# Performance work log

Hardware: AMD Instinct MI355X
Metric: run time of the kernel (lower is better)

The kernel has to match this reference:

```python
import jax, jax.numpy as jnp
import numpy as np

B, D, S, K, A = 4096, 256, 32, 8192, 256
BETA = 0.25  # vq_commitment_beta


def _ln(x, g, b):
    m = jnp.mean(x, axis=-1, keepdims=True)
    v = jnp.var(x, axis=-1, keepdims=True)
    return (x - m) * jax.lax.rsqrt(v + 1e-5) * g + b


def _clin(zr, zi, Wr, Wi, br, bi):
    # torch ComplexLinear: real = Wr(zr) - Wi(zi); imag = Wi(zr) + Wr(zi)
    return (zr @ Wr.T + br) - (zi @ Wi.T + bi), (zr @ Wi.T + bi) + (zi @ Wr.T + br)


def _forward(x_t_r, x_t_i, gw_r, gw_i, mem_r, mem_i, input_gate, vq_emb,
             vis_pal, aud_pal, mem_gate_W, mem_gate_b, mem_addr_W, mem_addr_b,
             mn_gr, mn_br, mn_gi, mn_bi,
             gq_Wr, gq_Wi, gq_br, gq_bi, gk_Wr, gk_Wi, gk_br, gk_bi,
             gv_Wr, gv_Wi, gv_br, gv_bi, sp_Wr, sp_Wi, sp_br, sp_bi,
             cr_Wr, cr_Wi, cr_br, cr_bi):
    # input gate blend (forward_step preamble)
    alpha = jax.nn.sigmoid(input_gate)
    gr = alpha * gw_r + (1.0 - alpha) * x_t_r
    gi = alpha * gw_i + (1.0 - alpha) * x_t_i
    z_flat = jnp.concatenate([gr, gi], -1)  # [B, 2D]

    # ---- EMA_VQ (eval path): cdist + argmin + straight-through ----
    d2 = (jnp.sum(z_flat ** 2, 1, keepdims=True) + jnp.sum(vq_emb ** 2, 1)
          - 2.0 * (z_flat @ vq_emb.T))  # [B, K]
    idx = jnp.argmin(d2, -1)
    z_q = vq_emb[idx]
    vq_loss = BETA * jnp.mean((jax.lax.stop_gradient(z_q) - z_flat) ** 2, -1)
    v_out = z_flat + jax.lax.stop_gradient(z_q - z_flat)
    probs = jnp.mean(jax.nn.one_hot(idx, K, dtype=jnp.float32), 0)
    batch_ent = -jnp.sum(probs * jnp.log(probs + 1e-10)) / jnp.log(jnp.asarray(K, jnp.float32))

    # ---- HermitianGating ----
    qr, qi = _clin(gr, gi, gq_Wr, gq_Wi, gq_br, gq_bi)
    kr, ki = _clin(gr, gi, gk_Wr, gk_Wi, gk_br, gk_bi)
    vr, vi = _clin(gr, gi, gv_Wr, gv_Wi, gv_br, gv_bi)
    gate = jax.nn.sigmoid(jnp.sum(qr * kr + qi * ki, -1, keepdims=True))  # Re(q k*)
    g_out = jnp.concatenate([vr * gate, vi * gate], -1)

    # ---- AssociativeMemory: content read + gated soft-scatter write ----
    sim = jnp.einsum('bsd,bd->bs', mem_r, gr) + jnp.einsum('bsd,bd->bs', mem_i, gi)  # Re(mem* q)
    attn = jax.nn.softmax(sim, -1)
    read_r = jnp.einsum('bs,bsd->bd', attn, mem_r)
    read_i = jnp.einsum('bs,bsd->bd', attn, mem_i)
    m_out = jnp.concatenate([read_r, read_i], -1)
    wgate = jax.nn.sigmoid(z_flat @ mem_gate_W.T + mem_gate_b)  # [B,1]
    ww = jax.nn.softmax(z_flat @ mem_addr_W.T + mem_addr_b, -1)  # [B,S]
    slot_ent = jnp.mean(-jnp.sum(ww * jnp.log(ww + 1e-10), -1))
    eff = wgate[:, :, None] * ww[:, :, None]  # [B,S,1]
    nm_r = _ln((1.0 - eff) * mem_r + eff * gr[:, None, :], mn_gr, mn_br)
    nm_i = _ln((1.0 - eff) * mem_i + eff * gi[:, None, :], mn_gi, mn_bi)

    # ---- HebbianSensory palette attention ----
    sr, si = _clin(gr, gi, sp_Wr, sp_Wi, sp_br, sp_bi)
    zf2 = jnp.concatenate([sr, si], -1)
    vis_attn = jax.nn.softmax(zf2 @ vis_pal.T, -1)
    aud_attn = jax.nn.softmax(zf2 @ aud_pal.T, -1)
    vis = vis_attn @ vis_pal
    aud = aud_attn @ aud_pal
    # experience = vis_c + i*aud_c
    s_out = jnp.concatenate([vis[:, :D] - aud[:, D:], vis[:, D:] + aud[:, :D]], -1)

    # ---- Critic: i * ComplexLinear(z) ----
    c_r, c_i = _clin(gr, gi, cr_Wr, cr_Wi, cr_br, cr_bi)
    c_out = jnp.concatenate([-c_i, c_r], -1)

    out_main = jnp.stack([v_out, g_out, m_out, s_out, c_out], 1)  # [B,5,2D]
    return out_main, nm_r, nm_i, idx, vq_loss, batch_ent, slot_ent


def setup_inputs():
    key = jax.random.key(0)
    ks = iter(jax.random.split(key, 48))
    n = lambda shape, s=1.0: jax.random.normal(next(ks), shape, dtype=jnp.float32) * s
    inp = {
        'x_t_r': n((B, D)), 'x_t_i': n((B, D)),
        'gw_r': n((B, D)), 'gw_i': n((B, D)),
        'mem_r': n((B, S, D)), 'mem_i': n((B, S, D)),
        'input_gate': jnp.zeros((), jnp.float32),
        'vq_emb': jax.random.uniform(next(ks), (K, 2 * D), jnp.float32, -1.0 / np.sqrt(D), 1.0 / np.sqrt(D)),
        'vis_pal': n((A, 2 * D)), 'aud_pal': n((A, 2 * D)),
        'mem_gate_W': n((1, 2 * D), 0.02), 'mem_gate_b': jnp.zeros((1,), jnp.float32),
        'mem_addr_W': n((S, 2 * D), 0.02), 'mem_addr_b': jnp.zeros((S,), jnp.float32),
        'mn_gr': jnp.ones((D,), jnp.float32), 'mn_br': jnp.zeros((D,), jnp.float32),
        'mn_gi': jnp.ones((D,), jnp.float32), 'mn_bi': jnp.zeros((D,), jnp.float32),
    }
    for p in ('gq', 'gk', 'gv', 'sp', 'cr'):
        inp[p + '_Wr'] = n((D, D), 0.05)
        inp[p + '_Wi'] = n((D, D), 0.05)
        inp[p + '_br'] = jnp.zeros((D,), jnp.float32)
        inp[p + '_bi'] = jnp.zeros((D,), jnp.float32)
    return inp


def reference(x_t_r, x_t_i, gw_r, gw_i, mem_r, mem_i, input_gate, vq_emb,
              vis_pal, aud_pal, mem_gate_W, mem_gate_b, mem_addr_W, mem_addr_b,
              mn_gr, mn_br, mn_gi, mn_bi,
              gq_Wr, gq_Wi, gq_br, gq_bi, gk_Wr, gk_Wi, gk_br, gk_bi,
              gv_Wr, gv_Wi, gv_br, gv_bi, sp_Wr, sp_Wi, sp_br, sp_bi,
              cr_Wr, cr_Wi, cr_br, cr_bi):
    return _forward(x_t_r, x_t_i, gw_r, gw_i, mem_r, mem_i, input_gate, vq_emb,
                    vis_pal, aud_pal, mem_gate_W, mem_gate_b, mem_addr_W, mem_addr_b,
                    mn_gr, mn_br, mn_gi, mn_bi,
                    gq_Wr, gq_Wi, gq_br, gq_bi, gk_Wr, gk_Wi, gk_br, gk_bi,
                    gv_Wr, gv_Wi, gv_br, gv_bi, sp_Wr, sp_Wi, sp_br, sp_bi,
                    cr_Wr, cr_Wi, cr_br, cr_bi)
```

## Files before the change

### kernel.cpp

```cpp
#include <hip/hip_runtime.h>
#include <hip/hip_bf16.h>
#include <math.h>

#define BN 4096
#define DN 256
#define SN 32
#define KN 8192
#define AN 256
#define TWO_D 512

typedef unsigned short ushort;
using bf16x8 = __attribute__((ext_vector_type(8))) short;
using f32x4  = __attribute__((ext_vector_type(4))) float;

#define OUT_MAIN 0ull
#define OUT_NMR  10485760ull
#define OUT_NMI  44040192ull
#define OUT_IDX  77594624ull
#define OUT_VQL  77598720ull
#define OUT_BENT 77602816ull
#define OUT_SENT 77602817ull

#define MBYTE (1024ull*1024ull)
#define WS_GR    (0ull)
#define WS_GI    (4ull*MBYTE)
#define WS_Z2H   (8ull*MBYTE)
#define WS_Z2L   (12ull*MBYTE)
#define WS_EH    (16ull*MBYTE)
#define WS_EL    (24ull*MBYTE)
#define WS_E2    (32ull*MBYTE)
#define WS_WBIG  (33ull*MBYTE)
#define WS_BIAS  (36ull*MBYTE)
#define WS_PALC  (37ull*MBYTE)
#define WS_VIST  (38ull*MBYTE)
#define WS_AUDT  (39ull*MBYTE)
#define WS_PVAL  (40ull*MBYTE)
#define WS_PIDX  (42ull*MBYTE)
#define WS_HIST  (44ull*MBYTE)
#define WS_ENTV  (44ull*MBYTE + 128ull*1024ull)
#define WS_CL    (45ull*MBYTE)
#define WS_LOGIT (65ull*MBYTE)
#define WS_ATTN  (73ull*MBYTE)
#define WS_VIS   (77ull*MBYTE)
#define WS_AUD   (85ull*MBYTE)

#define DEVINL __device__ __forceinline__

DEVINL ushort f2bf(float f) {
    union { float f; unsigned u; } v; v.f = f;
    unsigned r = v.u + 0x7fffu + ((v.u >> 16) & 1u);
    return (ushort)(r >> 16);
}
DEVINL float bf2f(ushort h) {
    union { unsigned u; float f; } v; v.u = ((unsigned)h) << 16;
    return v.f;
}
DEVINL float sigmoidf_(float x) { return 1.f / (1.f + __expf(-x)); }

__global__ __launch_bounds__(256) void k_prep_vq(const float* __restrict__ emb,
                                                 ushort* __restrict__ eh,
                                                 ushort* __restrict__ el,
                                                 float* __restrict__ e2) {
    int t = threadIdx.x, w = t >> 6, lane = t & 63;
    int row = blockIdx.x * 4 + w;
    const float* er = emb + (size_t)row * 512;
    float acc = 0.f;
    #pragma unroll
    for (int j = 0; j < 8; j++) {
        int k = lane + 64 * j;
        float e = er[k];
        ushort h = f2bf(e);
        eh[(size_t)row * 512 + k] = h;
        el[(size_t)row * 512 + k] = f2bf(e - bf2f(h));
        acc += e * e;
    }
    for (int m = 1; m < 64; m <<= 1) acc += __shfl_xor(acc, m, 64);
    if (lane == 0) e2[row] = acc;
}

__global__ void k_prep_wbig(const float* __restrict__ Wr, const float* __restrict__ Wi,
                            const float* __restrict__ br, const float* __restrict__ bi,
                            ushort* __restrict__ Wb, float* __restrict__ bias) {
    int idx = blockIdx.x * 256 + threadIdx.x;
    int j = idx >> 9, k = idx & 511;
    int part = j >> 8, jj = j & 255;
    float v;
    if (part == 0) v = (k < 256) ? Wr[jj * 256 + k] : -Wi[jj * 256 + (k - 256)];
    else           v = (k < 256) ? Wi[jj * 256 + k] :  Wr[jj * 256 + (k - 256)];
    Wb[idx] = f2bf(v);
    if (k == 0) bias[j] = part ? (br[jj] + bi[jj]) : (br[jj] - bi[jj]);
}

__global__ void k_prep_palcat(const float* __restrict__ vis, const float* __restrict__ aud,
                              ushort* __restrict__ palc) {
    int idx = blockIdx.x * 256 + threadIdx.x;
    int a = idx >> 9, k = idx & 511;
    float v = (a < 256) ? vis[a * 512 + k] : aud[(a - 256) * 512 + k];
    palc[idx] = f2bf(v);
}
__global__ void k_prep_palT(const float* __restrict__ vis, const float* __restrict__ aud,
                            ushort* __restrict__ visT, ushort* __restrict__ audT) {
    int idx = blockIdx.x * 256 + threadIdx.x;
    int j = idx >> 8, a = idx & 255;
    visT[j * 256 + a] = f2bf(vis[a * 512 + j]);
    audT[j * 256 + a] = f2bf(aud[a * 512 + j]);
}

__global__ void k_gate(const float* __restrict__ xr, const float* __restrict__ xi,
                       const float* __restrict__ gwr, const float* __restrict__ gwi,
                       const float* __restrict__ ig,
                       float* __restrict__ gr, float* __restrict__ gi,
                       ushort* __restrict__ z2h, ushort* __restrict__ z2l) {
    int i = blockIdx.x * 256 + threadIdx.x;
    float a = sigmoidf_(ig[0]);
    float r  = a * gwr[i] + (1.f - a) * xr[i];
    float im = a * gwi[i] + (1.f - a) * xi[i];
    gr[i] = r; gi[i] = im;
    int b = i >> 8, d = i & 255;
    size_t z = (size_t)b * 512;
    ushort rh = f2bf(r);  z2h[z + d] = rh;       z2l[z + d] = f2bf(r - bf2f(rh));
    ushort ih = f2bf(im); z2h[z + 256 + d] = ih; z2l[z + 256 + d] = f2bf(im - bf2f(ih));
}

__global__ __launch_bounds__(256) void k_vq_gemm(
    const ushort* __restrict__ Zh, const ushort* __restrict__ Zl,
    const ushort* __restrict__ Eh, const ushort* __restrict__ El,
    const float* __restrict__ e2, float* __restrict__ pval, int* __restrict__ pidx) {
    __shared__ ushort Ah[128 * 40], Al[128 * 40], Bh[128 * 40], Bl[128 * 40];
    const int m0 = blockIdx.y * 128, n0 = blockIdx.x * 128;
    const int t = threadIdx.x;
    const int w = t >> 6, lane = t & 63, q = lane >> 4, ln = lane & 15;
    const int wm = w >> 1, wn = w & 1;
    f32x4 acc[4][4] = {};
    const int lrow = t >> 2, lcol = (t & 3) * 8;
    for (int k0 = 0; k0 < 512; k0 += 32) {
        __syncthreads();
        #pragma unroll
        for (int rep = 0; rep < 2; rep++) {
            int r = lrow + rep * 64;
            *(uint4*)(&Ah[r * 40 + lcol]) = *(const uint4*)(Zh + (size_t)(m0 + r) * 512 + k0 + lcol);
            *(uint4*)(&Al[r * 40 + lcol]) = *(const uint4*)(Zl + (size_t)(m0 + r) * 512 + k0 + lcol);
            *(uint4*)(&Bh[r * 40 + lcol]) = *(const uint4*)(Eh + (size_t)(n0 + r) * 512 + k0 + lcol);
            *(uint4*)(&Bl[r * 40 + lcol]) = *(const uint4*)(El + (size_t)(n0 + r) * 512 + k0 + lcol);
        }
        __syncthreads();
        bf16x8 ah[4], al[4], bh[4], bl[4];
        #pragma unroll
        for (int i = 0; i < 4; i++) {
            int ar = wm * 64 + i * 16 + ln;
            ah[i] = *(const bf16x8*)(&Ah[ar * 40 + q * 8]);
            al[i] = *(const bf16x8*)(&Al[ar * 40 + q * 8]);
            int br = wn * 64 + i * 16 + ln;
            bh[i] = *(const bf16x8*)(&Bh[br * 40 + q * 8]);
            bl[i] = *(const bf16x8*)(&Bl[br * 40 + q * 8]);
        }
        #pragma unroll
        for (int i = 0; i < 4; i++)
            #pragma unroll
            for (int j = 0; j < 4; j++) {
                acc[i][j] = __builtin_amdgcn_mfma_f32_16x16x32_bf16(ah[i], bh[j], acc[i][j], 0, 0, 0);
                acc[i][j] = __builtin_amdgcn_mfma_f32_16x16x32_bf16(ah[i], bl[j], acc[i][j], 0, 0, 0);
                acc[i][j] = __builtin_amdgcn_mfma_f32_16x16x32_bf16(al[i], bh[j], acc[i][j], 0, 0, 0);
            }
    }
    float e2v[4]; int cidx[4];
    #pragma unroll
    for (int j = 0; j < 4; j++) { cidx[j] = n0 + wn * 64 + j * 16 + ln; e2v[j] = e2[cidx[j]]; }
    #pragma unroll
    for (int i = 0; i < 4; i++) {
        #pragma unroll
        for (int reg = 0; reg < 4; reg++) {
            float bv = 3.4e38f; int bc = 0x7fffffff;
            #pragma unroll
            for (int j = 0; j < 4; j++) {
                float s = e2v[j] - 2.f * acc[i][j][reg];
                if (s < bv || (s == bv && cidx[j] < bc)) { bv = s; bc = cidx[j]; }
            }
            for (int m = 1; m < 16; m <<= 1) {
                float ov = __shfl_xor(bv, m, 64);
                int   oc = __shfl_xor(bc, m, 64);
                if (ov < bv || (ov == bv && oc < bc)) { bv = ov; bc = oc; }
            }
            if (ln == 0) {
                int r = m0 + wm * 64 + i * 16 + q * 4 + reg;
                int slot = blockIdx.x * 2 + wn;
                pval[(size_t)r * 128 + slot] = bv;
                pidx[(size_t)r * 128 + slot] = bc;
            }
        }
    }
}

__global__ __launch_bounds__(256) void k_vqfin(
    const float* __restrict__ pval, const int* __restrict__ pidx,
    const float* __restrict__ emb, const float* __restrict__ gr,
    const float* __restrict__ gi, float* __restrict__ out, int* __restrict__ hist) {
    __shared__ float sz[512];
    __shared__ float sv[128];
    __shared__ int   scd[128];
    __shared__ int   topc[8];
    __shared__ double tsc[8];
    __shared__ int   sbc;
    int b = blockIdx.x, t = threadIdx.x;
    sz[t]       = gr[(size_t)b * 256 + t];
    sz[256 + t] = gi[(size_t)b * 256 + t];
    if (t < 128) { sv[t] = pval[(size_t)b * 128 + t]; scd[t] = pidx[(size_t)b * 128 + t]; }
    __syncthreads();
    if (t == 0) {
        for (int j = 0; j < 8; j++) {
            float bv = 3.4e38f; int bi = 0;
            for (int m = 0; m < 128; m++) {
                float v = sv[m];
                if (v < bv || (v == bv && scd[m] < scd[bi])) { bv = v; bi = m; }
            }
            topc[j] = scd[bi];
            sv[bi] = 3.4e38f;
        }
    }
    __syncthreads();
    int w = t >> 6, lane = t & 63;
    for (int rep = 0; rep < 2; rep++) {
        int j = w + rep * 4;
        int c = topc[j];
        const float* e = emb + (size_t)c * 512;
        double acc = 0.0;
        #pragma unroll
        for (int u = 0; u < 8; u++) {
            int k2 = lane + u * 64;
            double d = (double)sz[k2] - (double)e[k2];
            acc += d * d;
        }
        for (int m = 1; m < 64; m <<= 1) acc += __shfl_xor(acc, m, 64);
        if (lane == 0) tsc[j] = acc;
    }
    __syncthreads();
    if (t == 0) {
        double bv = tsc[0]; int bc = topc[0];
        for (int j = 1; j < 8; j++)
            if (tsc[j] < bv || (tsc[j] == bv && topc[j] < bc)) { bv = tsc[j]; bc = topc[j]; }
        sbc = bc;
        out[OUT_IDX + b] = (float)bc;
        out[OUT_VQL + b] = (float)(0.25 * bv / 512.0);
        atomicAdd(&hist[bc], 1);
    }
    __syncthreads();
    const float* e = emb + (size_t)sbc * 512;
    float* om = out + (size_t)b * 2560;
    om[t]       = e[t];
    om[256 + t] = e[256 + t];
}

__global__ __launch_bounds__(256) void k_gemm(
    const ushort* __restrict__ A, int lda,
    const ushort* __restrict__ Bm, int ldb,
    void* __restrict__ C, int ldc,
    int Kd, const float* __restrict__ bias, int obf) {
    __shared__ ushort As[128 * 40], Bs[128 * 40];
    const int m0 = blockIdx.y * 128, n0 = blockIdx.x * 128;
    const int t = threadIdx.x;
    const int w = t >> 6, lane = t & 63, q = lane >> 4, ln = lane & 15;
    const int wm = w >> 1, wn = w & 1;
    f32x4 acc[4][4] = {};
    const int lrow = t >> 2, lcol = (t & 3) * 8;
    for (int k0 = 0; k0 < Kd; k0 += 32) {
        __syncthreads();
        #pragma unroll
        for (int rep = 0; rep < 2; rep++) {
            int r = lrow + rep * 64;
            *(uint4*)(&As[r * 40 + lcol]) = *(const uint4*)(A + (size_t)(m0 + r) * lda + k0 + lcol);
            *(uint4*)(&Bs[r * 40 + lcol]) = *(const uint4*)(Bm + (size_t)(n0 + r) * ldb + k0 + lcol);
        }
        __syncthreads();
        bf16x8 af[4], bfr[4];
        #pragma unroll
        for (int i = 0; i < 4; i++) {
            af[i]  = *(const bf16x8*)(&As[(wm * 64 + i * 16 + ln) * 40 + q * 8]);
            bfr[i] = *(const bf16x8*)(&Bs[(wn * 64 + i * 16 + ln) * 40 + q * 8]);
        }
        #pragma unroll
        for (int i = 0; i < 4; i++)
            #pragma unroll
            for (int j = 0; j < 4; j++)
                acc[i][j] = __builtin_amdgcn_mfma_f32_16x16x32_bf16(af[i], bfr[j], acc[i][j], 0, 0, 0);
    }
    #pragma unroll
    for (int i = 0; i < 4; i++) {
        int r = m0 + wm * 64 + i * 16 + q * 4;
        #pragma unroll
        for (int j = 0; j < 4; j++) {
            int c = n0 + wn * 64 + j * 16 + ln;
            float bb = bias ? bias[c] : 0.f;
            #pragma unroll
            for (int reg = 0; reg < 4; reg++) {
                float v = acc[i][j][reg] + bb;
                if (obf) ((ushort*)C)[(size_t)(r + reg) * ldc + c] = f2bf(v);
                else     ((float*)C)[(size_t)(r + reg) * ldc + c] = v;
            }
        }
    }
}

__global__ __launch_bounds__(256) void k_hermit(const ushort* __restrict__ CL,
                                                float* __restrict__ out) {
    int b = blockIdx.x, t = threadIdx.x;
    const ushort* row = CL + (size_t)b * 2560;
    float qr = bf2f(row[t]), qi = bf2f(row[256 + t]);
    float kr = bf2f(row[512 + t]), ki = bf2f(row[768 + t]);
    float part = qr * kr + qi * ki;
    __shared__ float red[4];
    for (int m = 1; m < 64; m <<= 1) part += __shfl_xor(part, m, 64);
    if ((t & 63) == 0) red[t >> 6] = part;
    __syncthreads();
    float gate = sigmoidf_(red[0] + red[1] + red[2] + red[3]);
    float vr = bf2f(row[1024 + t]), vi = bf2f(row[1280 + t]);
    float* om = out + (size_t)b * 2560;
    om[512 + t] = vr * gate; om[512 + 256 + t] = vi * gate;
    float crr = bf2f(row[2048 + t]), cii = bf2f(row[2304 + t]);
    om[4 * 512 + t] = -cii; om[4 * 512 + 256 + t] = crr;
}

__global__ __launch_bounds__(256) void k_smax(const float* __restrict__ L,
                                              ushort* __restrict__ attn) {
    int b = blockIdx.x, t = threadIdx.x;
    __shared__ float sred[8];
    for (int h = 0; h < 2; h++) {
        float x = L[(size_t)b * 512 + h * 256 + t];
        float mx = x;
        for (int m = 1; m < 64; m <<= 1) mx = fmaxf(mx, __shfl_xor(mx, m, 64));
        if ((t & 63) == 0) sred[t >> 6] = mx;
        __syncthreads();
        mx = fmaxf(fmaxf(sred[0], sred[1]), fmaxf(sred[2], sred[3]));
        float e = __expf(x - mx);
        float su = e;
        for (int m = 1; m < 64; m <<= 1) su += __shfl_xor(su, m, 64);
        if ((t & 63) == 0) sred[4 + (t >> 6)] = su;
        __syncthreads();
        su = sred[4] + sred[5] + sred[6] + sred[7];
        attn[(size_t)b * 512 + h * 256 + t] = f2bf(e / su);
        __syncthreads();
    }
}

__global__ void k_sout(const float* __restrict__ vis, const float* __restrict__ aud,
                       float* __restrict__ out) {
    int i = blockIdx.x * 256 + threadIdx.x;
    int b = i >> 8, d = i & 255;
    const float* v = vis + (size_t)b * 512;
    const float* a = aud + (size_t)b * 512;
    float* om = out + (size_t)b * 2560 + 3 * 512;
    om[d]       = v[d] - a[256 + d];
    om[256 + d] = v[256 + d] + a[d];
}

DEVINL void ln_half(float (&v)[32], float zz,
                    const float* __restrict__ gam, const float* __restrict__ bet,
                    float* __restrict__ obase, int t, int wp, int hs,
                    float (*redA)[33], float (*redB)[33],
                    float* __restrict__ smn, float* __restrict__ srs,
                    const float* __restrict__ seff) {
    float keepU = 0.f, keepQ = 0.f;
    #pragma unroll
    for (int s = 0; s < 32; s++) {
        float eff = seff[s];
        float x = v[s] + eff * (zz - v[s]);
        v[s] = x;
        float su = x, sq = x * x;
        #pragma unroll
        for (int m = 1; m <= 16; m <<= 1) {
            su += __shfl_xor(su, m, 64);
            sq += __shfl_xor(sq, m, 64);
        }
        if (hs == s) { keepU = su; keepQ = sq; }
    }
    redA[wp][hs] = keepU;
    redB[wp][hs] = keepQ;
    __syncthreads();
    if (t < 32) {
        float su = 0.f, sq = 0.f;
        #pragma unroll
        for (int j = 0; j < 8; j++) { su += redA[j][t]; sq += redB[j][t]; }
        float mn = su * (1.f / 256.f);
        float va = sq * (1.f / 256.f) - mn * mn;
        smn[t] = mn; srs[t] = rsqrtf(va + 1e-5f);
    }
    __syncthreads();
    float gv = gam[t], bv = bet[t];
    #pragma unroll
    for (int s = 0; s < 32; s++)
        obase[(size_t)s * 256 + t] = (v[s] - smn[s]) * srs[s] * gv + bv;
    __syncthreads();
}

__global__ __launch_bounds__(256, 4) void k_mem(
    const float* __restrict__ mem_r, const float* __restrict__ mem_i,
    const float* __restrict__ gr, const float* __restrict__ gi,
    const float* __restrict__ gateW, const float* __restrict__ gateB,
    const float* __restrict__ addrW, const float* __restrict__ addrB,
    const float* __restrict__ mgr, const float* __restrict__ mbr,
    const float* __restrict__ mgi, const float* __restrict__ mbi,
    float* __restrict__ out, float* __restrict__ entv) {
    __shared__ float redA[8][33];
    __shared__ float redB[8][33];
    __shared__ float redG[8];
    __shared__ float satt[32], seff[32], smn[32], srs[32];
    const int b = blockIdx.x, t = threadIdx.x;
    const int w = t >> 6, lane = t & 63;
    const int wp = (w << 1) | (lane >> 5);
    const int hs = lane & 31;
    const float* mr = mem_r + (size_t)b * 8192;
    const float* mi = mem_i + (size_t)b * 8192;
    const float zr = gr[(size_t)b * 256 + t];
    const float zi = gi[(size_t)b * 256 + t];

    float vr_[32], vi_[32];
    #pragma unroll
    for (int s = 0; s < 32; s++) vr_[s] = mr[s * 256 + t];
    #pragma unroll
    for (int s = 0; s < 32; s++) vi_[s] = mi[s * 256 + t];

    {
        float keepS = 0.f;
        #pragma unroll
        for (int s = 0; s < 32; s++) {
            float ps = vr_[s] * zr + vi_[s] * zi;
            #pragma unroll
            for (int m = 1; m <= 16; m <<= 1) ps += __shfl_xor(ps, m, 64);
            if (hs == s) keepS = ps;
        }
        redA[wp][hs] = keepS;
    }
    {
        float keepW = 0.f;
        #pragma unroll 4
        for (int s = 0; s < 32; s++) {
            float pw = addrW[s * 512 + t] * zr + addrW[s * 512 + 256 + t] * zi;
            #pragma unroll
            for (int m = 1; m <= 16; m <<= 1) pw += __shfl_xor(pw, m, 64);
            if (hs == s) keepW = pw;
        }
        redB[wp][hs] = keepW;
    }
    {
        float pg = gateW[t] * zr + gateW[256 + t] * zi;
        #pragma unroll
        for (int m = 1; m <= 16; m <<= 1) pg += __shfl_xor(pg, m, 64);
        if (hs == 0) redG[wp] = pg;
    }
    __syncthreads();

    if (t < 32) {
        float sim = 0.f, wwl = addrB[t], g = gateB[0];
        #pragma unroll
        for (int j = 0; j < 8; j++) { sim += redA[j][t]; wwl += redB[j][t]; g += redG[j]; }
        float wg = sigmoidf_(g);
        float mx = sim;
        #pragma unroll
        for (int m = 1; m <= 16; m <<= 1) mx = fmaxf(mx, __shfl_xor(mx, m, 64));
        float e = __expf(sim - mx), su = e;
        #pragma unroll
        for (int m = 1; m <= 16; m <<= 1) su += __shfl_xor(su, m, 64);
        satt[t] = e / su;
        mx = wwl;
        #pragma unroll
        for (int m = 1; m <= 16; m <<= 1) mx = fmaxf(mx, __shfl_xor(mx, m, 64));
        e = __expf(wwl - mx); su = e;
        #pragma unroll
        for (int m = 1; m <= 16; m <<= 1) su += __shfl_xor(su, m, 64);
        float wv = e / su;
        seff[t] = wg * wv;
        float ent = -wv * __logf(wv + 1e-10f);
        #pragma unroll
        for (int m = 1; m <= 16; m <<= 1) ent += __shfl_xor(ent, m, 64);
        if (t == 0) entv[b] = ent;
    }
    __syncthreads();

    {
        float rr = 0.f, ri = 0.f;
        #pragma unroll
        for (int s = 0; s < 32; s++) { float a = satt[s]; rr += a * vr_[s]; ri += a * vi_[s]; }
        float* om = out + (size_t)b * 2560 + 1024;
        om[t] = rr; om[256 + t] = ri;
    }

    ln_half(vr_, zr, mgr, mbr, out + OUT_NMR + (size_t)b * 8192,
            t, wp, hs, redA, redB, smn, srs, seff);
    ln_half(vi_, zi, mgi, mbi, out + OUT_NMI + (size_t)b * 8192,
            t, wp, hs, redA, redB, smn, srs, seff);
}

__global__ __launch_bounds__(256) void k_scalars(const int* __restrict__ hist,
                                                 const float* __restrict__ entv,
                                                 float* __restrict__ out) {
    int t = threadIdx.x;
    float local = 0.f;
    for (int k = t; k < 8192; k += 256) {
        float p = (float)hist[k] * (1.f / 4096.f);
        local += -p * __logf(p + 1e-10f);
    }
    float se = 0.f;
    for (int k = t; k < 4096; k += 256) se += entv[k];
    __shared__ float red[4], red2[4];
    for (int m = 1; m < 64; m <<= 1) {
        local += __shfl_xor(local, m, 64);
        se    += __shfl_xor(se, m, 64);
    }
    if ((t & 63) == 0) { red[t >> 6] = local; red2[t >> 6] = se; }
    __syncthreads();
    if (t == 0) {
        float bent = (red[0] + red[1] + red[2] + red[3]) / logf(8192.f);
        out[OUT_BENT] = bent;
        out[OUT_SENT] = (red2[0] + red2[1] + red2[2] + red2[3]) * (1.f / 4096.f);
    }
}

extern "C" void kernel_launch(void* const* d_in, const int* in_sizes, int n_in,
                              void* d_out, int out_size, void* d_ws, size_t ws_size,
                              hipStream_t stream) {
    const float* x_t_r = (const float*)d_in[0];
    const float* x_t_i = (const float*)d_in[1];
    const float* gw_r  = (const float*)d_in[2];
    const float* gw_i  = (const float*)d_in[3];
    const float* mem_r = (const float*)d_in[4];
    const float* mem_i = (const float*)d_in[5];
    const float* ig    = (const float*)d_in[6];
    const float* emb   = (const float*)d_in[7];
    const float* visp  = (const float*)d_in[8];
    const float* audp  = (const float*)d_in[9];
    const float* gateW = (const float*)d_in[10];
    const float* gateB = (const float*)d_in[11];
    const float* addrW = (const float*)d_in[12];
    const float* addrB = (const float*)d_in[13];
    const float* mgr   = (const float*)d_in[14];
    const float* mbr   = (const float*)d_in[15];
    const float* mgi   = (const float*)d_in[16];
    const float* mbi   = (const float*)d_in[17];

    char* w = (char*)d_ws;
    float*  gr    = (float*)(w + WS_GR);
    float*  gi    = (float*)(w + WS_GI);
    ushort* z2h   = (ushort*)(w + WS_Z2H);
    ushort* z2l   = (ushort*)(w + WS_Z2L);
    ushort* eh    = (ushort*)(w + WS_EH);
    ushort* el    = (ushort*)(w + WS_EL);
    float*  e2    = (float*)(w + WS_E2);
    ushort* Wbig  = (ushort*)(w + WS_WBIG);
    float*  biasv = (float*)(w + WS_BIAS);
    ushort* palc  = (ushort*)(w + WS_PALC);
    ushort* visT  = (ushort*)(w + WS_VIST);
    ushort* audT  = (ushort*)(w + WS_AUDT);
    float*  pval  = (float*)(w + WS_PVAL);
    int*    pidx  = (int*)(w + WS_PIDX);
    int*    hist  = (int*)(w + WS_HIST);
    float*  entv  = (float*)(w + WS_ENTV);
    ushort* CLb   = (ushort*)(w + WS_CL);
    float*  logit = (float*)(w + WS_LOGIT);
    ushort* attn  = (ushort*)(w + WS_ATTN);
    float*  vis   = (float*)(w + WS_VIS);
    float*  aud   = (float*)(w + WS_AUD);
    float*  out   = (float*)d_out;

    hipMemsetAsync(w + WS_HIST, 0, 8192 * sizeof(int), stream);

    k_prep_vq<<<KN / 4, 256, 0, stream>>>(emb, eh, el, e2);
    for (int p = 0; p < 5; p++) {
        k_prep_wbig<<<1024, 256, 0, stream>>>(
            (const float*)d_in[18 + p * 4], (const float*)d_in[19 + p * 4],
            (const float*)d_in[20 + p * 4], (const float*)d_in[21 + p * 4],
            Wbig + (size_t)p * 512 * 512, biasv + p * 512);
    }
    k_prep_palcat<<<1024, 256, 0, stream>>>(visp, audp, palc);
    k_prep_palT<<<512, 256, 0, stream>>>(visp, audp, visT, audT);

    k_gate<<<BN, 256, 0, stream>>>(x_t_r, x_t_i, gw_r, gw_i, ig, gr, gi, z2h, z2l);

    k_vq_gemm<<<dim3(64, 32), 256, 0, stream>>>(z2h, z2l, eh, el, e2, pval, pidx);
    k_vqfin<<<BN, 256, 0, stream>>>(pval, pidx, emb, gr, gi, out, hist);

    k_gemm<<<dim3(20, 32), 256, 0, stream>>>(z2h, 512, Wbig, 512, CLb, 2560, 512, biasv, 1);
    k_hermit<<<BN, 256, 0, stream>>>(CLb, out);

    k_gemm<<<dim3(4, 32), 256, 0, stream>>>(CLb + 1536, 2560, palc, 512, logit, 512, 512, nullptr, 0);
    k_smax<<<BN, 256, 0, stream>>>(logit, attn);
    k_gemm<<<dim3(4, 32), 256, 0, stream>>>(attn, 512, visT, 256, vis, 512, 256, nullptr, 0);
    k_gemm<<<dim3(4, 32), 256, 0, stream>>>(attn + 256, 512, audT, 256, aud, 512, 256, nullptr, 0);
    k_sout<<<BN, 256, 0, stream>>>(vis, aud, out);

    k_mem<<<BN, 256, 0, stream>>>(mem_r, mem_i, gr, gi, gateW, gateB, addrW, addrB,
                                  mgr, mbr, mgi, mbi, out, entv);

    k_scalars<<<1, 256, 0, stream>>>(hist, entv, out);
}
```

Before: 1.071 ms.

## Replace per-slot butterfly reductions in k_mem with transposing fold32 reduction

Replaces the 32 independent 5-step shuffle reductions per slot with a recursive-halving transpose-fold that reduces 32 values across the wave in about 32 shuffles, leaving each lane holding one bit-reversed slot sum. Softmax, entropy and the layernorm statistics are then computed redundantly in every wave and broadcast with readlane, which removes the single-warp serial stage and one barrier per layernorm half. The aim is to cut shuffle count and synchronization in the memory-update kernel. In exchange it adds register pressure from the temp arrays and readlane-based indexing.

```diff
diff --git a/kernel.cpp b/kernel.cpp
--- a/kernel.cpp
+++ b/kernel.cpp
@@ -57,6 +57,28 @@
 }
 DEVINL float sigmoidf_(float x) { return 1.f / (1.f + __expf(-x)); }
 
+DEVINL int brev5(int x) {
+    return ((x & 1) << 4) | ((x & 2) << 2) | (x & 4) | ((x & 8) >> 2) | ((x & 16) >> 4);
+}
+DEVINL float rdlane(float v, int l) {
+    return __int_as_float(__builtin_amdgcn_readlane(__float_as_int(v), l));
+}
+DEVINL float fold32(float (&v)[32], int lane) {
+    #pragma unroll
+    for (int k = 0; k < 5; k++) {
+        const int half = 16 >> k;
+        const bool hi = (lane >> k) & 1;
+        #pragma unroll
+        for (int i = 0; i < half; i++) {
+            float send = hi ? v[i] : v[i + half];
+            float recv = __shfl_xor(send, 1 << k, 64);
+            float keep = hi ? v[i + half] : v[i];
+            v[i] = keep + recv;
+        }
+    }
+    return v[0] + __shfl_xor(v[0], 32, 64);
+}
+
 __global__ __launch_bounds__(256) void k_prep_vq(const float* __restrict__ emb,
                                                  ushort* __restrict__ eh,
                                                  ushort* __restrict__ el,
@@ -352,42 +374,42 @@
     om[256 + d] = v[256 + d] + a[d];
 }
 
-DEVINL void ln_half(float (&v)[32], float zz,
-                    const float* __restrict__ gam, const float* __restrict__ bet,
-                    float* __restrict__ obase, int t, int wp, int hs,
-                    float (*redA)[33], float (*redB)[33],
-                    float* __restrict__ smn, float* __restrict__ srs,
-                    const float* __restrict__ seff) {
-    float keepU = 0.f, keepQ = 0.f;
+DEVINL void ln_fold_half(const float (&v)[32], float zz, float eff,
+                         const float* __restrict__ gam, const float* __restrict__ bet,
+                         float* __restrict__ obase,
+                         int t, int w, int lane, int slot,
+                         float* __restrict__ redS, float* __restrict__ redW) {
+    float tmp[32];
     #pragma unroll
     for (int s = 0; s < 32; s++) {
-        float eff = seff[s];
-        float x = v[s] + eff * (zz - v[s]);
-        v[s] = x;
-        float su = x, sq = x * x;
-        #pragma unroll
-        for (int m = 1; m <= 16; m <<= 1) {
-            su += __shfl_xor(su, m, 64);
-            sq += __shfl_xor(sq, m, 64);
-        }
-        if (hs == s) { keepU = su; keepQ = sq; }
-    }
-    redA[wp][hs] = keepU;
-    redB[wp][hs] = keepQ;
-    __syncthreads();
-    if (t < 32) {
-        float su = 0.f, sq = 0.f;
-        #pragma unroll
-        for (int j = 0; j < 8; j++) { su += redA[j][t]; sq += redB[j][t]; }
-        float mn = su * (1.f / 256.f);
-        float va = sq * (1.f / 256.f) - mn * mn;
-        smn[t] = mn; srs[t] = rsqrtf(va + 1e-5f);
-    }
-    __syncthreads();
+        float e = rdlane(eff, brev5(s));
+        float x = v[s] + e * (zz - v[s]);
+        tmp[s] = x * x;
+    }
+    float sqp = fold32(tmp, lane);
+    if (lane < 32) redW[slot * 4 + w] = sqp;
+    #pragma unroll
+    for (int s = 0; s < 32; s++) {
+        float e = rdlane(eff, brev5(s));
+        tmp[s] = v[s] + e * (zz - v[s]);
+    }
+    float sup = fold32(tmp, lane);
+    if (lane < 32) redS[slot * 4 + w] = sup;
+    __syncthreads();
+    float4 u4 = *(const float4*)&redS[slot * 4];
+    float4 q4 = *(const float4*)&redW[slot * 4];
+    float mn = (u4.x + u4.y + u4.z + u4.w) * (1.f / 256.f);
+    float va = (q4.x + q4.y + q4.z + q4.w) * (1.f / 256.f) - mn * mn;
+    float rs = rsqrtf(va + 1e-5f);
     float gv = gam[t], bv = bet[t];
     #pragma unroll
-    for (int s = 0; s < 32; s++)
-        obase[(size_t)s * 256 + t] = (v[s] - smn[s]) * srs[s] * gv + bv;
+    for (int s = 0; s < 32; s++) {
+        float e  = rdlane(eff, brev5(s));
+        float m_ = rdlane(mn,  brev5(s));
+        float r_ = rdlane(rs,  brev5(s));
+        float x = v[s] + e * (zz - v[s]);
+        obase[(size_t)s * 256 + t] = (x - m_) * r_ * gv + bv;
+    }
     __syncthreads();
 }
 
@@ -399,14 +421,12 @@
     const float* __restrict__ mgr, const float* __restrict__ mbr,
     const float* __restrict__ mgi, const float* __restrict__ mbi,
     float* __restrict__ out, float* __restrict__ entv) {
-    __shared__ float redA[8][33];
-    __shared__ float redB[8][33];
-    __shared__ float redG[8];
-    __shared__ float satt[32], seff[32], smn[32], srs[32];
+    __shared__ __align__(16) float redS[128];
+    __shared__ __align__(16) float redW[128];
+    __shared__ __align__(16) float redG[4];
     const int b = blockIdx.x, t = threadIdx.x;
     const int w = t >> 6, lane = t & 63;
-    const int wp = (w << 1) | (lane >> 5);
-    const int hs = lane & 31;
+    const int slot = brev5(lane & 31);
     const float* mr = mem_r + (size_t)b * 8192;
     const float* mi = mem_i + (size_t)b * 8192;
     const float zr = gr[(size_t)b * 256 + t];
@@ -418,75 +438,73 @@
     #pragma unroll
     for (int s = 0; s < 32; s++) vi_[s] = mi[s * 256 + t];
 
+    float tmp[32];
+    #pragma unroll
+    for (int s = 0; s < 32; s++) tmp[s] = vr_[s] * zr + vi_[s] * zi;
     {
-        float keepS = 0.f;
-        #pragma unroll
-        for (int s = 0; s < 32; s++) {
-            float ps = vr_[s] * zr + vi_[s] * zi;
-            #pragma unroll
-            for (int m = 1; m <= 16; m <<= 1) ps += __shfl_xor(ps, m, 64);
-            if (hs == s) keepS = ps;
-        }
-        redA[wp][hs] = keepS;
-    }
+        float sp = fold32(tmp, lane);
+        if (lane < 32) redS[slot * 4 + w] = sp;
+    }
+    #pragma unroll 8
+    for (int s = 0; s < 32; s++)
+        tmp[s] = addrW[s * 512 + t] * zr + addrW[s * 512 + 256 + t] * zi;
     {
-        float keepW = 0.f;
-        #pragma unroll 4
-        for (int s = 0; s < 32; s++) {
-            float pw = addrW[s * 512 + t] * zr + addrW[s * 512 + 256 + t] * zi;
-            #pragma unroll
-            for (int m = 1; m <= 16; m <<= 1) pw += __shfl_xor(pw, m, 64);
-            if (hs == s) keepW = pw;
-        }
-        redB[wp][hs] = keepW;
+        float wp2 = fold32(tmp, lane);
+        if (lane < 32) redW[slot * 4 + w] = wp2;
     }
     {
         float pg = gateW[t] * zr + gateW[256 + t] * zi;
         #pragma unroll
-        for (int m = 1; m <= 16; m <<= 1) pg += __shfl_xor(pg, m, 64);
-        if (hs == 0) redG[wp] = pg;
-    }
-    __syncthreads();
-
-    if (t < 32) {
-        float sim = 0.f, wwl = addrB[t], g = gateB[0];
-        #pragma unroll
-        for (int j = 0; j < 8; j++) { sim += redA[j][t]; wwl += redB[j][t]; g += redG[j]; }
-        float wg = sigmoidf_(g);
-        float mx = sim;
-        #pragma unroll
-        for (int m = 1; m <= 16; m <<= 1) mx = fmaxf(mx, __shfl_xor(mx, m, 64));
-        float e = __expf(sim - mx), su = e;
-        #pragma unroll
-        for (int m = 1; m <= 16; m <<= 1) su += __shfl_xor(su, m, 64);
-        satt[t] = e / su;
-        mx = wwl;
-        #pragma unroll
-        for (int m = 1; m <= 16; m <<= 1) mx = fmaxf(mx, __shfl_xor(mx, m, 64));
-        e = __expf(wwl - mx); su = e;
-        #pragma unroll
-        for (int m = 1; m <= 16; m <<= 1) su += __shfl_xor(su, m, 64);
-        float wv = e / su;
-        seff[t] = wg * wv;
-        float ent = -wv * __logf(wv + 1e-10f);
-        #pragma unroll
-        for (int m = 1; m <= 16; m <<= 1) ent += __shfl_xor(ent, m, 64);
-        if (t == 0) entv[b] = ent;
-    }
-    __syncthreads();
+        for (int m = 1; m < 64; m <<= 1) pg += __shfl_xor(pg, m, 64);
+        if (lane == 0) redG[w] = pg;
+    }
+    __syncthreads();
+
+    float4 s4 = *(const float4*)&redS[slot * 4];
+    float4 w4 = *(const float4*)&redW[slot * 4];
+    float4 g4 = *(const float4*)&redG[0];
+    float simt = s4.x + s4.y + s4.z + s4.w;
+    float wwt  = w4.x + w4.y + w4.z + w4.w + addrB[slot];
+    float wg   = sigmoidf_(g4.x + g4.y + g4.z + g4.w + gateB[0]);
+    float mx = simt;
+    #pragma unroll
+    for (int m = 1; m <= 16; m <<= 1) mx = fmaxf(mx, __shfl_xor(mx, m, 64));
+    float att = __expf(simt - mx);
+    float su = att;
+    #pragma unroll
+    for (int m = 1; m <= 16; m <<= 1) su += __shfl_xor(su, m, 64);
+    att /= su;
+    mx = wwt;
+    #pragma unroll
+    for (int m = 1; m <= 16; m <<= 1) mx = fmaxf(mx, __shfl_xor(mx, m, 64));
+    float wv = __expf(wwt - mx);
+    su = wv;
+    #pragma unroll
+    for (int m = 1; m <= 16; m <<= 1) su += __shfl_xor(su, m, 64);
+    wv /= su;
+    float eff = wg * wv;
+    float ent = -wv * __logf(wv + 1e-10f);
+    #pragma unroll
+    for (int m = 1; m <= 16; m <<= 1) ent += __shfl_xor(ent, m, 64);
+    if (t == 0) entv[b] = ent;
 
     {
         float rr = 0.f, ri = 0.f;
         #pragma unroll
-        for (int s = 0; s < 32; s++) { float a = satt[s]; rr += a * vr_[s]; ri += a * vi_[s]; }
+        for (int c = 0; c < 32; c++) {
+            float a = rdlane(att, c);
+            rr += a * vr_[brev5(c)];
+            ri += a * vi_[brev5(c)];
+        }
         float* om = out + (size_t)b * 2560 + 1024;
         om[t] = rr; om[256 + t] = ri;
     }
-
-    ln_half(vr_, zr, mgr, mbr, out + OUT_NMR + (size_t)b * 8192,
-            t, wp, hs, redA, redB, smn, srs, seff);
-    ln_half(vi_, zi, mgi, mbi, out + OUT_NMI + (size_t)b * 8192,
-            t, wp, hs, redA, redB, smn, srs, seff);
+    __syncthreads();
+
+    ln_fold_half(vr_, zr, eff, mgr, mbr, out + OUT_NMR + (size_t)b * 8192,
+                 t, w, lane, slot, redS, redW);
+    ln_fold_half(vi_, zi, eff, mgi, mbi, out + OUT_NMI + (size_t)b * 8192,
+                 t, w, lane, slot, redS, redW);
 }
 
 __global__ __launch_bounds__(256) void k_scalars(const int* __restrict__ hist,
```

Measured after the change: 1.598 ms. 49.2% more time.
